# Performance work log

Measured on AMD Instinct MI355X. Metric: run time of the kernel, lower is better.

## Reference

```python
import jax, jax.numpy as jnp
import numpy as np

D_MODEL, D_FF = 1024, 4096
B, T = 4, 2048
K = 614  # int(d_ff * 0.15)


def setup_inputs() -> dict:
    key = jax.random.key(0)
    k1, k2, k3, k4 = jax.random.split(key, 4)
    s_in = 1.0 / np.sqrt(D_MODEL)
    s_ff = 1.0 / np.sqrt(D_FF)
    x = jax.random.normal(k1, (B, T, D_MODEL), jnp.float32)
    # torch nn.Linear default init: U(-1/sqrt(fan_in), 1/sqrt(fan_in)); weight shape [out, in]
    W1 = jax.random.uniform(k2, (D_FF, D_MODEL), jnp.float32, -s_in, s_in)
    W2 = jax.random.uniform(k3, (D_FF, D_MODEL), jnp.float32, -s_in, s_in)
    Wo = jax.random.uniform(k4, (D_MODEL, D_FF), jnp.float32, -s_ff, s_ff)
    return {"x": x, "W1": W1, "W2": W2, "Wo": Wo, "k": K}


def reference(x, W1, W2, Wo, k):
    gate = jnp.einsum('btd,fd->btf', x, W2)                 # [B,T,D_FF]
    act = jax.nn.silu(jnp.einsum('btd,fd->btf', x, W1))     # [B,T,D_FF]
    Bx, Tx, Dff = act.shape
    flat = act.reshape(Bx * Tx, Dff)
    _, topk_idx = jax.lax.top_k(flat, k)                    # [N, k]
    rows = jnp.arange(Bx * Tx)[:, None]
    mask = jnp.zeros_like(flat).at[rows, topk_idx].set(1.0).reshape(act.shape)
    sparse_act = act * mask                                  # eval-mode exact masking
    return jnp.einsum('btf,df->btd', sparse_act * gate, Wo)  # [B,T,D_MODEL]
```

## Files before the change

### kernel.cpp

```cpp
#include <hip/hip_runtime.h>
#include <stdint.h>

#define DEV __device__ __forceinline__

using f32x4  = __attribute__((ext_vector_type(4))) float;
using bf16x8 = __attribute__((ext_vector_type(8))) short;
typedef unsigned short u16;
typedef unsigned int   u32;

typedef const __attribute__((address_space(1))) void* gptr_t;
typedef __attribute__((address_space(3))) void*       lptr_t;

DEV u16 f2bf(float f) {
  union { float f; u32 u; } v; v.f = f;
  u32 lsb = (v.u >> 16) & 1u;
  v.u += 0x7fffu + lsb;
  return (u16)(v.u >> 16);
}
DEV float bf2f(u16 h) {
  union { u32 u; float f; } v; v.u = ((u32)h) << 16;
  return v.f;
}
DEV void async16(void* lds, const void* g) {
  __builtin_amdgcn_global_load_lds((gptr_t)(uintptr_t)g,
                                   (lptr_t)(u32)(uintptr_t)lds, 16, 0, 0);
}
DEV u32 fkey(float v) {
  u32 u = __float_as_uint(v);
  return u ^ ((u & 0x80000000u) ? 0xFFFFFFFFu : 0x80000000u);
}
DEV float unfkey(u32 key) {
  const u32 ub = (key & 0x80000000u) ? (key ^ 0x80000000u) : ~key;
  return __uint_as_float(ub);
}

__global__ __launch_bounds__(256) void split1_kernel(const float* __restrict__ src,
                                                     u16* __restrict__ hi, int n) {
  int i = blockIdx.x * 256 + threadIdx.x;
  if (i >= n) return;
  hi[i] = f2bf(src[i]);
}

DEV void swz_block(int& bx, int& by) {
  const int gx = gridDim.x, nwg = gx * gridDim.y;
  const int lid = by * gx + bx;
  const int cpx = nwg >> 3;
  const int swz = (lid & 7) * cpx + (lid >> 3);
  bx = swz % gx; by = swz / gx;
}

__global__ __launch_bounds__(512, 2) void gemm8p_kernel(
    const u16* __restrict__ A, const u16* __restrict__ B,
    float* __restrict__ C, int N, int K)
{
  __shared__ u16 smem[65536];

  const int tid  = threadIdx.x;
  const int lane = tid & 63;
  const int wid  = tid >> 6;
  const int wm = wid >> 2, wn = wid & 3;
  int bx = blockIdx.x, by = blockIdx.y;
  swz_block(bx, by);
  const int m0 = by * 256, n0 = bx * 256;
  const int nTiles = K >> 6;
  const int nIter  = K >> 7;

  f32x4 acc[8][4] = {};
  bf16x8 afr[4][2], bfr[2][2];

  auto stageHT = [&](int ab, int buf, int half, int ktile) {
    const int kt = ktile < nTiles ? ktile : nTiles - 1;
    const int k0 = kt << 6;
    const u16* __restrict__ src = ab ? B : A;
    const int g0 = (ab ? n0 : m0) + half * 128;
    const int baseu = ((buf * 2 + ab) * 2 + half) * 8192;
#pragma unroll
    for (int L = 0; L < 2; ++L) {
      const int s = L * 512 + tid;
      const int r = s >> 3, cs = s & 7;
      const int csg = cs ^ (r & 7);
      async16(smem + baseu + (L * 512 + (tid & ~63)) * 8,
              src + (size_t)(g0 + r) * K + k0 + csg * 8);
    }
  };
  auto ldA = [&](int buf, int mi, int ks) -> bf16x8 {
    const int rA = wm * 128 + mi * 16 + (lane & 15);
    const int h = rA >> 7, rl = rA & 127;
    const int cs = (ks * 4 + (lane >> 4)) ^ (rl & 7);
    return *(const bf16x8*)&smem[((buf * 2 + 0) * 2 + h) * 8192 + rl * 64 + cs * 8];
  };
  auto ldB = [&](int buf, int ni, int ks) -> bf16x8 {
    const int rB = wn * 64 + ni * 16 + (lane & 15);
    const int h = rB >> 7, rl = rB & 127;
    const int cs = (ks * 4 + (lane >> 4)) ^ (rl & 7);
    return *(const bf16x8*)&smem[((buf * 2 + 1) * 2 + h) * 8192 + rl * 64 + cs * 8];
  };

  stageHT(0, 0, 0, 0); stageHT(0, 0, 1, 0);
  stageHT(1, 0, 0, 0); stageHT(1, 0, 1, 0);
  asm volatile("s_waitcnt vmcnt(0)" ::: "memory");
  __builtin_amdgcn_sched_barrier(0);
  __builtin_amdgcn_s_barrier();
  __builtin_amdgcn_sched_barrier(0);

  for (int i = 0; i < nIter; ++i) {
    const int t2 = 2 * i;
#pragma unroll
    for (int p = 0; p < 8; ++p) {
      const int pm = p & 3, bufC = p >> 2;
      const int miB = (pm >> 1) * 4, niB = (pm & 1) * 2;
      if ((pm & 1) == 0) {
#pragma unroll
        for (int m = 0; m < 4; ++m)
#pragma unroll
          for (int ks = 0; ks < 2; ++ks)
            afr[m][ks] = ldA(bufC, miB + m, ks);
      }
#pragma unroll
      for (int n = 0; n < 2; ++n)
#pragma unroll
        for (int ks = 0; ks < 2; ++ks)
          bfr[n][ks] = ldB(bufC, niB + n, ks);
      if (p == 0)      { stageHT(0, 1, 0, t2 + 1); stageHT(0, 1, 1, t2 + 1); }
      else if (p == 1) { stageHT(1, 1, 0, t2 + 1); stageHT(1, 1, 1, t2 + 1); }
      else if (p == 4) { stageHT(0, 0, 0, t2 + 2); stageHT(0, 0, 1, t2 + 2); }
      else if (p == 5) { stageHT(1, 0, 0, t2 + 2); stageHT(1, 0, 1, t2 + 2); }
      __builtin_amdgcn_sched_barrier(0);
      __builtin_amdgcn_s_barrier();
      __builtin_amdgcn_sched_barrier(0);
      __builtin_amdgcn_s_setprio(1);
#pragma unroll
      for (int m = 0; m < 4; ++m)
#pragma unroll
        for (int n = 0; n < 2; ++n)
#pragma unroll
          for (int ks = 0; ks < 2; ++ks)
            acc[miB + m][niB + n] = __builtin_amdgcn_mfma_f32_16x16x32_bf16(
                afr[m][ks], bfr[n][ks], acc[miB + m][niB + n], 0, 0, 0);
      __builtin_amdgcn_s_setprio(0);
      if (pm == 3)
        asm volatile("s_waitcnt vmcnt(0)" ::: "memory");
      __builtin_amdgcn_sched_barrier(0);
      __builtin_amdgcn_s_barrier();
      __builtin_amdgcn_sched_barrier(0);
    }
  }
  asm volatile("s_waitcnt vmcnt(0)" ::: "memory");

#pragma unroll
  for (int mi = 0; mi < 8; ++mi) {
    const int rb = m0 + wm * 128 + mi * 16 + (lane >> 4) * 4;
#pragma unroll
    for (int ni = 0; ni < 4; ++ni) {
      const int col = n0 + wn * 64 + ni * 16 + (lane & 15);
#pragma unroll
      for (int r2 = 0; r2 < 4; ++r2)
        C[(size_t)(rb + r2) * N + col] = acc[mi][ni][r2];
    }
  }
}

template<int BK>
__global__ __launch_bounds__(256) void gemm_bt(
    const u16* __restrict__ A, const u16* __restrict__ B,
    float* __restrict__ C, int N, int K)
{
  constexpr int TILE = 128 * BK;
  __shared__ u16 smem[2 * TILE];
  u16* sA = smem;
  u16* sB = smem + TILE;

  const int tid  = threadIdx.x;
  const int lane = tid & 63;
  const int wave = tid >> 6;
  const int wr = wave >> 1, wc = wave & 1;
  int bx = blockIdx.x, by = blockIdx.y;
  swz_block(bx, by);
  const int m0 = by * 128, n0 = bx * 128;

  f32x4 acc[4][4] = {};
  constexpr int SPR   = BK / 8;
  constexpr int ITERS = (128 * SPR) / 256;

  for (int k0 = 0; k0 < K; k0 += BK) {
#pragma unroll
    for (int i = 0; i < ITERS; ++i) {
      const int slot = i * 256 + tid;
      const int r = slot / SPR, cc = slot % SPR;
      const int uni = (i * 256 + wave * 64) * 8;
      async16(sA + uni, A + (size_t)(m0 + r) * K + k0 + cc * 8);
      async16(sB + uni, B + (size_t)(n0 + r) * K + k0 + cc * 8);
    }
    __syncthreads();

#pragma unroll
    for (int ks = 0; ks < BK / 32; ++ks) {
      const int kb = ks * 32 + (lane >> 4) * 8;
      bf16x8 a[4], b[4];
#pragma unroll
      for (int i = 0; i < 4; ++i) {
        a[i] = *(const bf16x8*)&sA[(wr * 64 + i * 16 + (lane & 15)) * BK + kb];
        b[i] = *(const bf16x8*)&sB[(wc * 64 + i * 16 + (lane & 15)) * BK + kb];
      }
#pragma unroll
      for (int mi = 0; mi < 4; ++mi)
#pragma unroll
        for (int ni = 0; ni < 4; ++ni)
          acc[mi][ni] = __builtin_amdgcn_mfma_f32_16x16x32_bf16(a[mi], b[ni], acc[mi][ni], 0, 0, 0);
    }
    __syncthreads();
  }

#pragma unroll
  for (int mi = 0; mi < 4; ++mi) {
    const int rbase = m0 + wr * 64 + mi * 16 + (lane >> 4) * 4;
#pragma unroll
    for (int ni = 0; ni < 4; ++ni) {
      const int col = n0 + wc * 64 + ni * 16 + (lane & 15);
#pragma unroll
      for (int r2 = 0; r2 < 4; ++r2)
        C[(size_t)(rbase + r2) * N + col] = acc[mi][ni][r2];
    }
  }
}

__global__ __launch_bounds__(256) void select7_kernel(
    const float* __restrict__ zg, const float* __restrict__ xin,
    const float* __restrict__ W1,
    u16* __restrict__ sbuf, const int* __restrict__ kptr)
{
  const int row = blockIdx.x, tid = threadIdx.x;
  const int lane = tid & 63, wave = tid >> 6;
  const int k = *kptr;

  __shared__ float xrow[1024];
  __shared__ float sact[4096];
  __shared__ unsigned char flag[4096];
  __shared__ int wsum[4];
  __shared__ int s_nb;
  __shared__ int band_idx[256];
  __shared__ u32 band_key[256];
  __shared__ float band_act[256];

  const float* zrow = zg + (size_t)row * 8192;
  const float* grow = zrow + 4096;

  float zreg[16];
#pragma unroll
  for (int q = 0; q < 4; ++q) {
    const float4 v = *(const float4*)&zrow[q * 1024 + tid * 4];
    zreg[q * 4 + 0] = v.x; zreg[q * 4 + 1] = v.y;
    zreg[q * 4 + 2] = v.z; zreg[q * 4 + 3] = v.w;
  }
  *(float4*)&xrow[tid * 4] = *(const float4*)&xin[(size_t)row * 1024 + tid * 4];
  *(u32*)&flag[tid * 4] = 0u;
  *(u32*)&flag[1024 + tid * 4] = 0u;
  *(u32*)&flag[2048 + tid * 4] = 0u;
  *(u32*)&flag[3072 + tid * 4] = 0u;
  if (tid == 0) s_nb = 0;
  __syncthreads();

  u32 prefix = 0;
  for (int step = 0; step < 20; ++step) {
    const u32 c = prefix | (1u << (31 - step));
    const float zc = unfkey(c);
    int cnt = 0;
#pragma unroll
    for (int i = 0; i < 16; ++i) cnt += (zreg[i] >= zc) ? 1 : 0;
    for (int off = 32; off; off >>= 1) cnt += __shfl_xor(cnt, off);
    if (lane == 0) wsum[wave] = cnt;
    __syncthreads();
    const int tot = wsum[0] + wsum[1] + wsum[2] + wsum[3];
    if (tot >= k) prefix = c;
    __syncthreads();
  }
  const float tau = unfkey(prefix);
  const float BANDW = 1.5e-2f;
  const float thi = tau + BANDW, tlo = tau - BANDW;

  int cntD = 0;
#pragma unroll
  for (int q = 0; q < 4; ++q)
#pragma unroll
    for (int j = 0; j < 4; ++j) {
      const int f = q * 1024 + tid * 4 + j;
      const float zv = zreg[q * 4 + j];
      if (zv > thi) { flag[f] = 1; ++cntD; }
      else if (zv >= tlo) {
        const int p = atomicAdd(&s_nb, 1);
        if (p < 256) band_idx[p] = f;
      }
    }
  for (int off = 32; off; off >>= 1) cntD += __shfl_xor(cntD, off);
  if (lane == 0) wsum[wave] = cntD;
  __syncthreads();
  const int D = wsum[0] + wsum[1] + wsum[2] + wsum[3];
  const int nb = (s_nb < 256) ? s_nb : 256;
  const int need = k - D;

  {
    const int gi = tid >> 2, l = tid & 3;
    const int wl = lane & ~3;
    for (int i = gi; i < nb; i += 64) {
      const int f = band_idx[i];
      const float* wr = W1 + (size_t)f * 1024;
      float v = 0.f;
#pragma unroll 8
      for (int b = 0; b < 1024; b += 16) {
        float t = __fadd_rn(__fmul_rn(xrow[b + 12 + l], wr[b + 12 + l]), v);
        t = __fadd_rn(__fmul_rn(xrow[b + 8 + l],  wr[b + 8 + l]),  t);
        t = __fadd_rn(__fmul_rn(xrow[b + 4 + l],  wr[b + 4 + l]),  t);
        v = __fadd_rn(__fmul_rn(xrow[b + 0 + l],  wr[b + 0 + l]),  t);
      }
      const float c0 = __shfl(v, wl + 0);
      const float c1 = __shfl(v, wl + 1);
      const float c2 = __shfl(v, wl + 2);
      const float c3 = __shfl(v, wl + 3);
      if (l == 0) {
        const float zrep = __fadd_rn(__fadd_rn(c0, c1), __fadd_rn(c2, c3));
        const double zd = (double)zrep;
        const float a = (float)(zd / (1.0 + exp(-zd)));
        band_act[i] = a;
        band_key[i] = fkey(a);
      }
    }
  }
  __syncthreads();

  for (int i = tid; i < nb; i += 256) {
    const u32 ki = band_key[i];
    const int fi = band_idx[i];
    int rank = 0;
    for (int j = 0; j < nb; ++j) {
      const u32 kj = band_key[j];
      rank += (kj > ki || (kj == ki && band_idx[j] < fi)) ? 1 : 0;
    }
    if (rank < need) { flag[fi] = 2; sact[fi] = band_act[i]; }
  }
  __syncthreads();

  u16* srow = sbuf + (size_t)row * 4096;
#pragma unroll
  for (int q = 0; q < 4; ++q) {
    const int f0 = q * 1024 + tid * 4;
    const float4 gv = *(const float4*)&grow[f0];
    const float gvv[4] = { gv.x, gv.y, gv.z, gv.w };
    const u32 fl = *(const u32*)&flag[f0];
    u16 out[4];
#pragma unroll
    for (int j = 0; j < 4; ++j) {
      const u32 fj = (fl >> (8 * j)) & 0xFF;
      float sval = 0.f;
      if (fj == 2) {
        sval = sact[f0 + j] * gvv[j];
      } else if (fj == 1) {
        const float zz = zreg[q * 4 + j];
        sval = (zz / (1.f + expf(-zz))) * gvv[j];
      }
      out[j] = f2bf(sval);
    }
    *(ushort4*)&srow[f0] = make_ushort4(out[0], out[1], out[2], out[3]);
  }
}

extern "C" void kernel_launch(void* const* d_in, const int* in_sizes, int n_in,
                              void* d_out, int out_size, void* d_ws, size_t ws_size,
                              hipStream_t stream)
{
  const float* x  = (const float*)d_in[0];
  const float* W1 = (const float*)d_in[1];
  const float* W2 = (const float*)d_in[2];
  const float* Wo = (const float*)d_in[3];
  const int* kptr = (const int*)d_in[4];

  const int DM = 1024, DF = 4096;
  const int M = in_sizes[0] / DM;
  const size_t nX = (size_t)M * DM, nW = (size_t)DF * DM, nWo = (size_t)DM * DF;

  char* w = (char*)d_ws;
  u16* x_hi   = (u16*)w;  w += nX * 2;
  u16* w12_hi = (u16*)w;  w += 2 * nW * 2;
  u16* wo_hi  = (u16*)w;  w += nWo * 2;
  const size_t fixed_bytes = (size_t)(w - (char*)d_ws);

  int nch = 1;
  while (nch < 64) {
    const size_t per = (size_t)(M / nch) * DF * 10;
    if (fixed_bytes + per <= ws_size) break;
    nch *= 2;
  }
  const int Mc = M / nch;

  float* zgbuf = (float*)w;
  u16*   sbuf  = (u16*)(w + (size_t)Mc * DF * 8);

  split1_kernel<<<dim3((int)((nX + 255) / 256)), 256, 0, stream>>>(x, x_hi, (int)nX);
  split1_kernel<<<dim3((int)((nW + 255) / 256)), 256, 0, stream>>>(W1, w12_hi, (int)nW);
  split1_kernel<<<dim3((int)((nW + 255) / 256)), 256, 0, stream>>>(W2, w12_hi + nW, (int)nW);
  split1_kernel<<<dim3((int)((nWo + 255) / 256)), 256, 0, stream>>>(Wo, wo_hi, (int)nWo);

  for (int ch = 0; ch < nch; ++ch) {
    const size_t ro = (size_t)ch * Mc;
    gemm8p_kernel<<<dim3(2 * DF / 256, Mc / 256), 512, 0, stream>>>(
        x_hi + ro * DM, w12_hi, zgbuf, 2 * DF, DM);
    select7_kernel<<<dim3(Mc), 256, 0, stream>>>(
        zgbuf, x + ro * DM, W1, sbuf, kptr);
    gemm_bt<64><<<dim3(DM / 128, Mc / 128), 256, 0, stream>>>(
        sbuf, wo_hi, (float*)d_out + ro * DM, DM, DF);
  }
}
```

Measured before the change: 694.3 us.

## Split W1 GEMM into 3-pass bf16x3 and narrow top-k refinement band

Computes the W1 pre-activation with a split-bf16 three-segment GEMM (hi*hi + hi*lo + lo*hi) so it is close to fp32, and runs a separate single-pass GEMM for the gate that writes bf16. The more accurate z lets the selection kernel shrink its tie-break band from 1.5e-2 to 8e-4, leaving far fewer band candidates that need exact recomputation from x and W1 and pairwise ranking. The cost is three times the MFMA work for the W1 half, extra hi/lo split kernels, and two GEMM launches instead of one fused 2*DF GEMM.

Result: faster. 647.4 us (-6.7%).

```diff
diff --git a/kernel.cpp b/kernel.cpp
--- a/kernel.cpp
+++ b/kernel.cpp
@@ -39,6 +39,15 @@
   int i = blockIdx.x * 256 + threadIdx.x;
   if (i >= n) return;
   hi[i] = f2bf(src[i]);
+}
+__global__ __launch_bounds__(256) void split2_kernel(const float* __restrict__ src,
+                                                     u16* __restrict__ hi, u16* __restrict__ lo, int n) {
+  int i = blockIdx.x * 256 + threadIdx.x;
+  if (i >= n) return;
+  float v = src[i];
+  u16 h = f2bf(v);
+  hi[i] = h;
+  lo[i] = f2bf(v - bf2f(h));
 }
 
 DEV void swz_block(int& bx, int& by) {
@@ -49,9 +58,11 @@
   bx = swz % gx; by = swz / gx;
 }
 
+template<int K, int NSEG, bool OUTBF16>
 __global__ __launch_bounds__(512, 2) void gemm8p_kernel(
-    const u16* __restrict__ A, const u16* __restrict__ B,
-    float* __restrict__ C, int N, int K)
+    const u16* __restrict__ A0, const u16* __restrict__ A1, const u16* __restrict__ A2,
+    const u16* __restrict__ B0, const u16* __restrict__ B1, const u16* __restrict__ B2,
+    void* __restrict__ Cout, int N)
 {
   __shared__ u16 smem[65536];
 
@@ -62,16 +73,20 @@
   int bx = blockIdx.x, by = blockIdx.y;
   swz_block(bx, by);
   const int m0 = by * 256, n0 = bx * 256;
-  const int nTiles = K >> 6;
-  const int nIter  = K >> 7;
+  constexpr int TPS    = K >> 6;
+  constexpr int nTiles = NSEG * TPS;
+  constexpr int nIter  = nTiles / 2;
 
   f32x4 acc[8][4] = {};
   bf16x8 afr[4][2], bfr[2][2];
 
   auto stageHT = [&](int ab, int buf, int half, int ktile) {
-    const int kt = ktile < nTiles ? ktile : nTiles - 1;
-    const int k0 = kt << 6;
-    const u16* __restrict__ src = ab ? B : A;
+    const int kt  = ktile < nTiles ? ktile : nTiles - 1;
+    const int seg = kt / TPS;
+    const int k0  = (kt - seg * TPS) << 6;
+    const u16* __restrict__ src =
+        ab ? (seg == 0 ? B0 : seg == 1 ? B1 : B2)
+           : (seg == 0 ? A0 : seg == 1 ? A1 : A2);
     const int g0 = (ab ? n0 : m0) + half * 128;
     const int baseu = ((buf * 2 + ab) * 2 + half) * 8192;
 #pragma unroll
@@ -154,8 +169,12 @@
     for (int ni = 0; ni < 4; ++ni) {
       const int col = n0 + wn * 64 + ni * 16 + (lane & 15);
 #pragma unroll
-      for (int r2 = 0; r2 < 4; ++r2)
-        C[(size_t)(rb + r2) * N + col] = acc[mi][ni][r2];
+      for (int r2 = 0; r2 < 4; ++r2) {
+        if constexpr (OUTBF16)
+          ((u16*)Cout)[(size_t)(rb + r2) * N + col] = f2bf(acc[mi][ni][r2]);
+        else
+          ((float*)Cout)[(size_t)(rb + r2) * N + col] = acc[mi][ni][r2];
+      }
     }
   }
 }
@@ -224,9 +243,9 @@
   }
 }
 
-__global__ __launch_bounds__(256) void select7_kernel(
-    const float* __restrict__ zg, const float* __restrict__ xin,
-    const float* __restrict__ W1,
+__global__ __launch_bounds__(256) void select9_kernel(
+    const float* __restrict__ z, const u16* __restrict__ g,
+    const float* __restrict__ xin, const float* __restrict__ W1,
     u16* __restrict__ sbuf, const int* __restrict__ kptr)
 {
   const int row = blockIdx.x, tid = threadIdx.x;
@@ -242,8 +261,8 @@
   __shared__ u32 band_key[256];
   __shared__ float band_act[256];
 
-  const float* zrow = zg + (size_t)row * 8192;
-  const float* grow = zrow + 4096;
+  const float* zrow = z + (size_t)row * 4096;
+  const u16*   grow = g + (size_t)row * 4096;
 
   float zreg[16];
 #pragma unroll
@@ -275,7 +294,7 @@
     __syncthreads();
   }
   const float tau = unfkey(prefix);
-  const float BANDW = 1.5e-2f;
+  const float BANDW = 8e-4f;
   const float thi = tau + BANDW, tlo = tau - BANDW;
 
   int cntD = 0;
@@ -343,8 +362,8 @@
 #pragma unroll
   for (int q = 0; q < 4; ++q) {
     const int f0 = q * 1024 + tid * 4;
-    const float4 gv = *(const float4*)&grow[f0];
-    const float gvv[4] = { gv.x, gv.y, gv.z, gv.w };
+    const ushort4 gu = *(const ushort4*)&grow[f0];
+    const float gvv[4] = { bf2f(gu.x), bf2f(gu.y), bf2f(gu.z), bf2f(gu.w) };
     const u32 fl = *(const u32*)&flag[f0];
     u16 out[4];
 #pragma unroll
@@ -378,34 +397,42 @@
   const size_t nX = (size_t)M * DM, nW = (size_t)DF * DM, nWo = (size_t)DM * DF;
 
   char* w = (char*)d_ws;
-  u16* x_hi   = (u16*)w;  w += nX * 2;
-  u16* w12_hi = (u16*)w;  w += 2 * nW * 2;
-  u16* wo_hi  = (u16*)w;  w += nWo * 2;
+  u16* x_hi  = (u16*)w;  w += nX * 2;
+  u16* x_lo  = (u16*)w;  w += nX * 2;
+  u16* W1_hi = (u16*)w;  w += nW * 2;
+  u16* W1_lo = (u16*)w;  w += nW * 2;
+  u16* W2_hi = (u16*)w;  w += nW * 2;
+  u16* Wo_hi = (u16*)w;  w += nWo * 2;
   const size_t fixed_bytes = (size_t)(w - (char*)d_ws);
 
   int nch = 1;
   while (nch < 64) {
-    const size_t per = (size_t)(M / nch) * DF * 10;
+    const size_t per = (size_t)(M / nch) * DF * 8;
     if (fixed_bytes + per <= ws_size) break;
     nch *= 2;
   }
   const int Mc = M / nch;
 
-  float* zgbuf = (float*)w;
-  u16*   sbuf  = (u16*)(w + (size_t)Mc * DF * 8);
-
-  split1_kernel<<<dim3((int)((nX + 255) / 256)), 256, 0, stream>>>(x, x_hi, (int)nX);
-  split1_kernel<<<dim3((int)((nW + 255) / 256)), 256, 0, stream>>>(W1, w12_hi, (int)nW);
-  split1_kernel<<<dim3((int)((nW + 255) / 256)), 256, 0, stream>>>(W2, w12_hi + nW, (int)nW);
-  split1_kernel<<<dim3((int)((nWo + 255) / 256)), 256, 0, stream>>>(Wo, wo_hi, (int)nWo);
+  float* zbuf = (float*)w;
+  u16*   gbuf = (u16*)(w + (size_t)Mc * DF * 4);
+  u16*   sbuf = (u16*)(w + (size_t)Mc * DF * 6);
+
+  split2_kernel<<<dim3((int)((nX + 255) / 256)), 256, 0, stream>>>(x, x_hi, x_lo, (int)nX);
+  split2_kernel<<<dim3((int)((nW + 255) / 256)), 256, 0, stream>>>(W1, W1_hi, W1_lo, (int)nW);
+  split1_kernel<<<dim3((int)((nW + 255) / 256)), 256, 0, stream>>>(W2, W2_hi, (int)nW);
+  split1_kernel<<<dim3((int)((nWo + 255) / 256)), 256, 0, stream>>>(Wo, Wo_hi, (int)nWo);
 
   for (int ch = 0; ch < nch; ++ch) {
     const size_t ro = (size_t)ch * Mc;
-    gemm8p_kernel<<<dim3(2 * DF / 256, Mc / 256), 512, 0, stream>>>(
-        x_hi + ro * DM, w12_hi, zgbuf, 2 * DF, DM);
-    select7_kernel<<<dim3(Mc), 256, 0, stream>>>(
-        zgbuf, x + ro * DM, W1, sbuf, kptr);
+    gemm8p_kernel<1024, 3, false><<<dim3(DF / 256, Mc / 256), 512, 0, stream>>>(
+        x_hi + ro * DM, x_hi + ro * DM, x_lo + ro * DM,
+        W1_hi, W1_lo, W1_hi, zbuf, DF);
+    gemm8p_kernel<1024, 1, true><<<dim3(DF / 256, Mc / 256), 512, 0, stream>>>(
+        x_hi + ro * DM, x_hi + ro * DM, x_hi + ro * DM,
+        W2_hi, W2_hi, W2_hi, gbuf, DF);
+    select9_kernel<<<dim3(Mc), 256, 0, stream>>>(
+        zbuf, gbuf, x + ro * DM, W1, sbuf, kptr);
     gemm_bt<64><<<dim3(DM / 128, Mc / 128), 256, 0, stream>>>(
-        sbuf, wo_hi, (float*)d_out + ro * DM, DM, DF);
-  }
-}
+        sbuf, Wo_hi, (float*)d_out + ro * DM, DM, DF);
+  }
+}
```
